# Kernel optimization log

Measured on AMD Instinct MI355X. Metric: run time of the kernel, lower is better.

The kernel has to match this reference:

```python
import jax, jax.numpy as jnp
import numpy as np


def _conv1x1(x, w, b):
    # x: [B, Cin, H, W]; w: [Cout, Cin, 1, 1]; b: [Cout]
    y = jnp.einsum('bchw,oc->bohw', x, w[:, :, 0, 0])
    return y + b[None, :, None, None]


def setup_inputs() -> dict:
    key = jax.random.key(0)
    ks = jax.random.split(key, 9)
    B, C, H, W = 8, 256, 64, 64
    Cq = C // 4
    sc = 0.05
    return {
        'x': jax.random.normal(ks[0], (B, C, H, W), jnp.float32),
        'query_weight': jax.random.normal(ks[1], (Cq, C, 1, 1), jnp.float32) * sc,
        'query_bias': jax.random.normal(ks[2], (Cq,), jnp.float32) * sc,
        'key_weight': jax.random.normal(ks[3], (Cq, C, 1, 1), jnp.float32) * sc,
        'key_bias': jax.random.normal(ks[4], (Cq,), jnp.float32) * sc,
        'value_weight': jax.random.normal(ks[5], (C, C, 1, 1), jnp.float32) * sc,
        'value_bias': jax.random.normal(ks[6], (C,), jnp.float32) * sc,
        'gamma_weight': jax.random.normal(ks[7], (C, C, 1, 1), jnp.float32) * sc,
        'gamma_bias': jax.random.normal(ks[8], (C,), jnp.float32) * sc,
    }


def reference(x, query_weight, query_bias, key_weight, key_bias,
              value_weight, value_bias, gamma_weight, gamma_bias):
    B, C, H, W = x.shape
    N = H * W
    q = _conv1x1(x, query_weight, query_bias).reshape(B, -1, N)   # [B, Cq, N]
    k = _conv1x1(x, key_weight, key_bias).reshape(B, -1, N)       # [B, Cq, N]
    v = _conv1x1(x, value_weight, value_bias).reshape(B, C, N)    # [B, C, N]
    # energy[b, i, j] = sum_c q[b, c, i] * k[b, c, j]
    energy = jnp.einsum('bci,bcj->bij', q, k)                     # [B, N, N]
    energy = jax.nn.elu(energy) / N
    out = jnp.einsum('bcn,bnm->bcm', v, energy).reshape(B, C, H, W)
    return _conv1x1(out, gamma_weight, gamma_bias)
```

## Files before the change

kernel.cpp:

```cpp
#include <hip/hip_runtime.h>
#include <cmath>

#define BB 8
#define CC 256
#define CQ 64
#define NN 4096
constexpr float INV_N = 1.0f / 4096.0f;

typedef __attribute__((ext_vector_type(8))) short short8;
typedef __attribute__((ext_vector_type(4))) short short4v;
typedef __attribute__((ext_vector_type(4))) float float4v;

__device__ __forceinline__ short f2bf(float f) {
  union { float f; unsigned u; } x; x.f = f;
  unsigned r = x.u + 0x7fffu + ((x.u >> 16) & 1u);
  return (short)(r >> 16);
}

__global__ __launch_bounds__(256, 2) void qkv_kernel(
    const float* __restrict__ X,
    const float* __restrict__ wq, const float* __restrict__ bq,
    const float* __restrict__ wk, const float* __restrict__ bk,
    const float* __restrict__ wv, const float* __restrict__ bv,
    short* __restrict__ qt, short* __restrict__ kt, short* __restrict__ vbf) {
  __shared__ short xt[64 * 272];
  __shared__ short Os[64 * 72];
  const int tid = threadIdx.x;
  const int wid = tid >> 6;
  const int lane = tid & 63, quad = lane >> 4, l16 = lane & 15;
  const int n0 = blockIdx.x * 64, b = blockIdx.y;

#pragma unroll 4
  for (int p = 0; p < 16; ++p) {
    const int idx = p * 256 + tid;
    const int c = idx >> 4;
    const int n4 = (idx & 15) * 4;
    const float4 x4 = *reinterpret_cast<const float4*>(
        &X[((size_t)b * CC + c) * NN + n0 + n4]);
    xt[(n4 + 0) * 272 + c] = f2bf(x4.x);
    xt[(n4 + 1) * 272 + c] = f2bf(x4.y);
    xt[(n4 + 2) * 272 + c] = f2bf(x4.z);
    xt[(n4 + 3) * 272 + c] = f2bf(x4.w);
  }
  __syncthreads();

  for (int ch = 0; ch < 6; ++ch) {
    const float* W; const float* bias; int obase;
    if (ch == 0)      { W = wq; bias = bq; obase = 0; }
    else if (ch == 1) { W = wk; bias = bk; obase = 0; }
    else { W = wv + (size_t)(ch - 2) * 64 * CC; bias = bv + (ch - 2) * 64; obase = (ch - 2) * 64; }

    float4v acc[4];
#pragma unroll
    for (int tm = 0; tm < 4; ++tm) acc[tm] = float4v{0.f, 0.f, 0.f, 0.f};

#pragma unroll
    for (int kk = 0; kk < 8; ++kk) {
      const float* wp = &W[(size_t)(wid * 16 + l16) * CC + kk * 32 + quad * 8];
      const float4v w0 = *reinterpret_cast<const float4v*>(wp);
      const float4v w1 = *reinterpret_cast<const float4v*>(wp + 4);
      short8 a;
      a[0] = f2bf(w0[0]); a[1] = f2bf(w0[1]); a[2] = f2bf(w0[2]); a[3] = f2bf(w0[3]);
      a[4] = f2bf(w1[0]); a[5] = f2bf(w1[1]); a[6] = f2bf(w1[2]); a[7] = f2bf(w1[3]);
#pragma unroll
      for (int tm = 0; tm < 4; ++tm) {
        const short8 bfrag = *reinterpret_cast<const short8*>(
            &xt[(tm * 16 + l16) * 272 + kk * 32 + quad * 8]);
        acc[tm] = __builtin_amdgcn_mfma_f32_16x16x32_bf16(a, bfrag, acc[tm], 0, 0, 0);
      }
    }

    if (ch < 2) {
      short* dst = (ch == 0) ? qt : kt;
#pragma unroll
      for (int tm = 0; tm < 4; ++tm) {
        short4v pk;
#pragma unroll
        for (int r = 0; r < 4; ++r)
          pk[r] = f2bf(acc[tm][r] + bias[wid * 16 + quad * 4 + r]);
        *reinterpret_cast<short4v*>(
            &dst[((size_t)b * NN + n0 + tm * 16 + l16) * 64 + wid * 16 + quad * 4]) = pk;
      }
    } else {
      __syncthreads();
#pragma unroll
      for (int tm = 0; tm < 4; ++tm)
#pragma unroll
        for (int r = 0; r < 4; ++r)
          Os[(wid * 16 + quad * 4 + r) * 72 + tm * 16 + l16] =
              f2bf(acc[tm][r] + bias[wid * 16 + quad * 4 + r]);
      __syncthreads();
      const int o = tid >> 2, ng = (tid & 3) * 16;
      const short8 s0 = *reinterpret_cast<const short8*>(&Os[o * 72 + ng]);
      const short8 s1 = *reinterpret_cast<const short8*>(&Os[o * 72 + ng + 8]);
      short* vp = &vbf[((size_t)b * CC + obase + o) * NN + n0 + ng];
      *reinterpret_cast<short8*>(vp) = s0;
      *reinterpret_cast<short8*>(vp + 8) = s1;
    }
  }
}

__global__ __launch_bounds__(256, 2) void attn_kernel(
    const short* __restrict__ qt, const short* __restrict__ kt,
    const short* __restrict__ vbf, const float* __restrict__ Wg,
    const float* __restrict__ bg, float* __restrict__ out) {
  __shared__ short smem[16896];
  short* Es0 = smem;
  short* Es1 = smem + 4608;
  short* Outs = smem;

  const int tid = threadIdx.x;
  const int wid = tid >> 6;
  const int lane = tid & 63, quad = lane >> 4, l16 = lane & 15;
  const int m0 = blockIdx.x * 64, b = blockIdx.y;

  short8 bkf[4][2];
#pragma unroll
  for (int tm = 0; tm < 4; ++tm)
#pragma unroll
    for (int kk = 0; kk < 2; ++kk)
      bkf[tm][kk] = *reinterpret_cast<const short8*>(
          &kt[((size_t)b * NN + m0 + tm * 16 + l16) * 64 + kk * 32 + quad * 8]);

  const short* qrow = &qt[((size_t)b * NN + wid * 16 + l16) * 64 + quad * 8];
  const short* vrow[4];
#pragma unroll
  for (int tc = 0; tc < 4; ++tc)
    vrow[tc] = &vbf[((size_t)b * CC + wid * 64 + tc * 16 + l16) * NN + quad * 8];

  float4v acc[4][4];
#pragma unroll
  for (int i = 0; i < 4; ++i)
#pragma unroll
    for (int j = 0; j < 4; ++j) acc[i][j] = float4v{0.f, 0.f, 0.f, 0.f};

  short8 aq0 = *reinterpret_cast<const short8*>(qrow);
  short8 aq1 = *reinterpret_cast<const short8*>(qrow + 32);

  for (int it = 0; it < 64; ++it) {
    const int nb = it * 64;
    short* Esw = (it & 1) ? Es1 : Es0;

    short8 av[4][2];
#pragma unroll
    for (int tc = 0; tc < 4; ++tc) {
      av[tc][0] = *reinterpret_cast<const short8*>(vrow[tc] + nb);
      av[tc][1] = *reinterpret_cast<const short8*>(vrow[tc] + nb + 32);
    }

    float4v s[4];
#pragma unroll
    for (int tm = 0; tm < 4; ++tm) {
      float4v t = {0.f, 0.f, 0.f, 0.f};
      t = __builtin_amdgcn_mfma_f32_16x16x32_bf16(aq0, bkf[tm][0], t, 0, 0, 0);
      t = __builtin_amdgcn_mfma_f32_16x16x32_bf16(aq1, bkf[tm][1], t, 0, 0, 0);
      s[tm] = t;
    }

    const short8 aq0n = *reinterpret_cast<const short8*>(qrow + (size_t)(it + 1) * 64 * 64);
    const short8 aq1n = *reinterpret_cast<const short8*>(qrow + (size_t)(it + 1) * 64 * 64 + 32);

#pragma unroll
    for (int tm = 0; tm < 4; ++tm) {
      short4v pk;
#pragma unroll
      for (int r = 0; r < 4; ++r) {
        float sv = s[tm][r];
        sv = (sv > 0.f) ? sv : (__expf(sv) - 1.f);
        pk[r] = f2bf(sv * INV_N);
      }
      *reinterpret_cast<short4v*>(
          &Esw[(tm * 16 + l16) * 72 + wid * 16 + quad * 4]) = pk;
    }
    __syncthreads();

#pragma unroll
    for (int tm = 0; tm < 4; ++tm) {
      const short8 be0 = *reinterpret_cast<const short8*>(
          &Esw[(tm * 16 + l16) * 72 + quad * 8]);
      const short8 be1 = *reinterpret_cast<const short8*>(
          &Esw[(tm * 16 + l16) * 72 + 32 + quad * 8]);
#pragma unroll
      for (int tc = 0; tc < 4; ++tc) {
        acc[tc][tm] = __builtin_amdgcn_mfma_f32_16x16x32_bf16(av[tc][0], be0, acc[tc][tm], 0, 0, 0);
        acc[tc][tm] = __builtin_amdgcn_mfma_f32_16x16x32_bf16(av[tc][1], be1, acc[tc][tm], 0, 0, 0);
      }
    }
    aq0 = aq0n; aq1 = aq1n;
  }

  __syncthreads();
#pragma unroll
  for (int tc = 0; tc < 4; ++tc)
#pragma unroll
    for (int tm = 0; tm < 4; ++tm) {
      short4v pk;
#pragma unroll
      for (int r = 0; r < 4; ++r) pk[r] = f2bf(acc[tc][tm][r]);
      *reinterpret_cast<short4v*>(
          &Outs[(tm * 16 + l16) * 264 + wid * 64 + tc * 16 + quad * 4]) = pk;
    }
  __syncthreads();

#pragma unroll
  for (int i = 0; i < 4; ++i)
#pragma unroll
    for (int j = 0; j < 4; ++j) acc[i][j] = float4v{0.f, 0.f, 0.f, 0.f};

  for (int ks8 = 0; ks8 < 8; ++ks8) {
    short8 ag[4];
#pragma unroll
    for (int to = 0; to < 4; ++to) {
      const float* wp =
          &Wg[(size_t)(wid * 64 + to * 16 + l16) * CC + ks8 * 32 + quad * 8];
      const float4v w0 = *reinterpret_cast<const float4v*>(wp);
      const float4v w1 = *reinterpret_cast<const float4v*>(wp + 4);
      short8 a;
      a[0] = f2bf(w0[0]); a[1] = f2bf(w0[1]); a[2] = f2bf(w0[2]); a[3] = f2bf(w0[3]);
      a[4] = f2bf(w1[0]); a[5] = f2bf(w1[1]); a[6] = f2bf(w1[2]); a[7] = f2bf(w1[3]);
      ag[to] = a;
    }
    short8 bo[4];
#pragma unroll
    for (int tm = 0; tm < 4; ++tm)
      bo[tm] = *reinterpret_cast<const short8*>(
          &Outs[(tm * 16 + l16) * 264 + ks8 * 32 + quad * 8]);
#pragma unroll
    for (int to = 0; to < 4; ++to)
#pragma unroll
      for (int tm = 0; tm < 4; ++tm)
        acc[to][tm] =
            __builtin_amdgcn_mfma_f32_16x16x32_bf16(ag[to], bo[tm], acc[to][tm], 0, 0, 0);
  }

#pragma unroll
  for (int to = 0; to < 4; ++to) {
#pragma unroll
    for (int r = 0; r < 4; ++r) {
      const int o = wid * 64 + to * 16 + quad * 4 + r;
      const float bgv = bg[o];
#pragma unroll
      for (int tm = 0; tm < 4; ++tm) {
        out[((size_t)b * CC + o) * NN + m0 + tm * 16 + l16] =
            acc[to][tm][r] + bgv;
      }
    }
  }
}

extern "C" void kernel_launch(void* const* d_in, const int* in_sizes, int n_in,
                              void* d_out, int out_size, void* d_ws,
                              size_t ws_size, hipStream_t stream) {
  const float* x  = (const float*)d_in[0];
  const float* wq = (const float*)d_in[1];
  const float* bq = (const float*)d_in[2];
  const float* wk = (const float*)d_in[3];
  const float* bk = (const float*)d_in[4];
  const float* wv = (const float*)d_in[5];
  const float* bv = (const float*)d_in[6];
  const float* wg = (const float*)d_in[7];
  const float* bg = (const float*)d_in[8];
  float* out = (float*)d_out;

  short* qt  = (short*)d_ws;
  short* kt  = qt + (size_t)BB * NN * CQ;
  short* vbf = kt + (size_t)BB * NN * CQ;

  qkv_kernel<<<dim3(NN / 64, BB), 256, 0, stream>>>(x, wq, bq, wk, bk, wv, bv,
                                                    qt, kt, vbf);
  attn_kernel<<<dim3(NN / 64, BB), 256, 0, stream>>>(qt, kt, vbf, wg, bg, out);
}
```

Baseline: 286.0 us.

## Pre-convert weights to bf16, prefetch V fragments, and swap grid axes

```diff
diff --git a/kernel.cpp b/kernel.cpp
--- a/kernel.cpp
+++ b/kernel.cpp
@@ -17,18 +17,38 @@
   return (short)(r >> 16);
 }
 
+__global__ void wconv_kernel(const float* __restrict__ wq,
+                             const float* __restrict__ wk,
+                             const float* __restrict__ wv,
+                             const float* __restrict__ wg,
+                             short* __restrict__ wqb, short* __restrict__ wkb,
+                             short* __restrict__ wvb, short* __restrict__ wgb) {
+  const int t = blockIdx.x * 256 + threadIdx.x;
+  const float* src;
+  short* dst;
+  int idx;
+  if (t < 4096)        { src = wq; dst = wqb; idx = t; }
+  else if (t < 8192)   { src = wk; dst = wkb; idx = t - 4096; }
+  else if (t < 24576)  { src = wv; dst = wvb; idx = t - 8192; }
+  else                 { src = wg; dst = wgb; idx = t - 24576; }
+  const float4 v = *reinterpret_cast<const float4*>(&src[(size_t)idx * 4]);
+  short4v o;
+  o[0] = f2bf(v.x); o[1] = f2bf(v.y); o[2] = f2bf(v.z); o[3] = f2bf(v.w);
+  *reinterpret_cast<short4v*>(&dst[(size_t)idx * 4]) = o;
+}
+
 __global__ __launch_bounds__(256, 2) void qkv_kernel(
     const float* __restrict__ X,
-    const float* __restrict__ wq, const float* __restrict__ bq,
-    const float* __restrict__ wk, const float* __restrict__ bk,
-    const float* __restrict__ wv, const float* __restrict__ bv,
+    const short* __restrict__ wqb, const float* __restrict__ bq,
+    const short* __restrict__ wkb, const float* __restrict__ bk,
+    const short* __restrict__ wvb, const float* __restrict__ bv,
     short* __restrict__ qt, short* __restrict__ kt, short* __restrict__ vbf) {
   __shared__ short xt[64 * 272];
   __shared__ short Os[64 * 72];
   const int tid = threadIdx.x;
   const int wid = tid >> 6;
   const int lane = tid & 63, quad = lane >> 4, l16 = lane & 15;
-  const int n0 = blockIdx.x * 64, b = blockIdx.y;
+  const int b = blockIdx.x, n0 = blockIdx.y * 64;
 
 #pragma unroll 4
   for (int p = 0; p < 16; ++p) {
@@ -45,29 +65,28 @@
   __syncthreads();
 
   for (int ch = 0; ch < 6; ++ch) {
-    const float* W; const float* bias; int obase;
-    if (ch == 0)      { W = wq; bias = bq; obase = 0; }
-    else if (ch == 1) { W = wk; bias = bk; obase = 0; }
-    else { W = wv + (size_t)(ch - 2) * 64 * CC; bias = bv + (ch - 2) * 64; obase = (ch - 2) * 64; }
+    const short* W; const float* bias; int obase;
+    if (ch == 0)      { W = wqb; bias = bq; obase = 0; }
+    else if (ch == 1) { W = wkb; bias = bk; obase = 0; }
+    else { W = wvb + (size_t)(ch - 2) * 64 * CC; bias = bv + (ch - 2) * 64; obase = (ch - 2) * 64; }
 
     float4v acc[4];
 #pragma unroll
     for (int tm = 0; tm < 4; ++tm) acc[tm] = float4v{0.f, 0.f, 0.f, 0.f};
 
+    const short* wrow = &W[(size_t)(wid * 16 + l16) * CC + quad * 8];
+    short8 a_cur = *reinterpret_cast<const short8*>(wrow);
 #pragma unroll
     for (int kk = 0; kk < 8; ++kk) {
-      const float* wp = &W[(size_t)(wid * 16 + l16) * CC + kk * 32 + quad * 8];
-      const float4v w0 = *reinterpret_cast<const float4v*>(wp);
-      const float4v w1 = *reinterpret_cast<const float4v*>(wp + 4);
-      short8 a;
-      a[0] = f2bf(w0[0]); a[1] = f2bf(w0[1]); a[2] = f2bf(w0[2]); a[3] = f2bf(w0[3]);
-      a[4] = f2bf(w1[0]); a[5] = f2bf(w1[1]); a[6] = f2bf(w1[2]); a[7] = f2bf(w1[3]);
+      short8 a_nxt = a_cur;
+      if (kk < 7) a_nxt = *reinterpret_cast<const short8*>(wrow + (kk + 1) * 32);
 #pragma unroll
       for (int tm = 0; tm < 4; ++tm) {
         const short8 bfrag = *reinterpret_cast<const short8*>(
             &xt[(tm * 16 + l16) * 272 + kk * 32 + quad * 8]);
-        acc[tm] = __builtin_amdgcn_mfma_f32_16x16x32_bf16(a, bfrag, acc[tm], 0, 0, 0);
-      }
+        acc[tm] = __builtin_amdgcn_mfma_f32_16x16x32_bf16(a_cur, bfrag, acc[tm], 0, 0, 0);
+      }
+      a_cur = a_nxt;
     }
 
     if (ch < 2) {
@@ -102,7 +121,7 @@
 
 __global__ __launch_bounds__(256, 2) void attn_kernel(
     const short* __restrict__ qt, const short* __restrict__ kt,
-    const short* __restrict__ vbf, const float* __restrict__ Wg,
+    const short* __restrict__ vbf, const short* __restrict__ wgb,
     const float* __restrict__ bg, float* __restrict__ out) {
   __shared__ short smem[16896];
   short* Es0 = smem;
@@ -112,7 +131,7 @@
   const int tid = threadIdx.x;
   const int wid = tid >> 6;
   const int lane = tid & 63, quad = lane >> 4, l16 = lane & 15;
-  const int m0 = blockIdx.x * 64, b = blockIdx.y;
+  const int b = blockIdx.x, m0 = blockIdx.y * 64;
 
   short8 bkf[4][2];
 #pragma unroll
@@ -136,16 +155,21 @@
 
   short8 aq0 = *reinterpret_cast<const short8*>(qrow);
   short8 aq1 = *reinterpret_cast<const short8*>(qrow + 32);
-
-  for (int it = 0; it < 64; ++it) {
-    const int nb = it * 64;
+  short8 av0[4][2], av1[4][2];
+#pragma unroll
+  for (int tc = 0; tc < 4; ++tc) {
+    av0[tc][0] = *reinterpret_cast<const short8*>(vrow[tc]);
+    av0[tc][1] = *reinterpret_cast<const short8*>(vrow[tc] + 32);
+  }
+
+  auto body = [&](int it, short8 (&avc)[4][2], short8 (&avn)[4][2]) {
     short* Esw = (it & 1) ? Es1 : Es0;
-
-    short8 av[4][2];
+    const int nbn = (it + 1) * 64;
+
 #pragma unroll
     for (int tc = 0; tc < 4; ++tc) {
-      av[tc][0] = *reinterpret_cast<const short8*>(vrow[tc] + nb);
-      av[tc][1] = *reinterpret_cast<const short8*>(vrow[tc] + nb + 32);
+      avn[tc][0] = *reinterpret_cast<const short8*>(vrow[tc] + nbn);
+      avn[tc][1] = *reinterpret_cast<const short8*>(vrow[tc] + nbn + 32);
     }
 
     float4v s[4];
@@ -157,8 +181,8 @@
       s[tm] = t;
     }
 
-    const short8 aq0n = *reinterpret_cast<const short8*>(qrow + (size_t)(it + 1) * 64 * 64);
-    const short8 aq1n = *reinterpret_cast<const short8*>(qrow + (size_t)(it + 1) * 64 * 64 + 32);
+    const short8 aq0n = *reinterpret_cast<const short8*>(qrow + (size_t)nbn * 64);
+    const short8 aq1n = *reinterpret_cast<const short8*>(qrow + (size_t)nbn * 64 + 32);
 
 #pragma unroll
     for (int tm = 0; tm < 4; ++tm) {
@@ -182,11 +206,16 @@
           &Esw[(tm * 16 + l16) * 72 + 32 + quad * 8]);
 #pragma unroll
       for (int tc = 0; tc < 4; ++tc) {
-        acc[tc][tm] = __builtin_amdgcn_mfma_f32_16x16x32_bf16(av[tc][0], be0, acc[tc][tm], 0, 0, 0);
-        acc[tc][tm] = __builtin_amdgcn_mfma_f32_16x16x32_bf16(av[tc][1], be1, acc[tc][tm], 0, 0, 0);
+        acc[tc][tm] = __builtin_amdgcn_mfma_f32_16x16x32_bf16(avc[tc][0], be0, acc[tc][tm], 0, 0, 0);
+        acc[tc][tm] = __builtin_amdgcn_mfma_f32_16x16x32_bf16(avc[tc][1], be1, acc[tc][tm], 0, 0, 0);
       }
     }
     aq0 = aq0n; aq1 = aq1n;
+  };
+
+  for (int it = 0; it < 64; it += 2) {
+    body(it, av0, av1);
+    body(it + 1, av1, av0);
   }
 
   __syncthreads();
@@ -210,16 +239,9 @@
   for (int ks8 = 0; ks8 < 8; ++ks8) {
     short8 ag[4];
 #pragma unroll
-    for (int to = 0; to < 4; ++to) {
-      const float* wp =
-          &Wg[(size_t)(wid * 64 + to * 16 + l16) * CC + ks8 * 32 + quad * 8];
-      const float4v w0 = *reinterpret_cast<const float4v*>(wp);
-      const float4v w1 = *reinterpret_cast<const float4v*>(wp + 4);
-      short8 a;
-      a[0] = f2bf(w0[0]); a[1] = f2bf(w0[1]); a[2] = f2bf(w0[2]); a[3] = f2bf(w0[3]);
-      a[4] = f2bf(w1[0]); a[5] = f2bf(w1[1]); a[6] = f2bf(w1[2]); a[7] = f2bf(w1[3]);
-      ag[to] = a;
-    }
+    for (int to = 0; to < 4; ++to)
+      ag[to] = *reinterpret_cast<const short8*>(
+          &wgb[(size_t)(wid * 64 + to * 16 + l16) * CC + ks8 * 32 + quad * 8]);
     short8 bo[4];
 #pragma unroll
     for (int tm = 0; tm < 4; ++tm)
@@ -265,8 +287,13 @@
   short* qt  = (short*)d_ws;
   short* kt  = qt + (size_t)BB * NN * CQ;
   short* vbf = kt + (size_t)BB * NN * CQ;
-
-  qkv_kernel<<<dim3(NN / 64, BB), 256, 0, stream>>>(x, wq, bq, wk, bk, wv, bv,
+  short* wqb = vbf + (size_t)BB * CC * NN;
+  short* wkb = wqb + (size_t)CQ * CC;
+  short* wvb = wkb + (size_t)CQ * CC;
+  short* wgb = wvb + (size_t)CC * CC;
+
+  wconv_kernel<<<dim3(160), 256, 0, stream>>>(wq, wk, wv, wg, wqb, wkb, wvb, wgb);
+  qkv_kernel<<<dim3(BB, NN / 64), 256, 0, stream>>>(x, wqb, bq, wkb, bk, wvb, bv,
                                                     qt, kt, vbf);
-  attn_kernel<<<dim3(NN / 64, BB), 256, 0, stream>>>(qt, kt, vbf, wg, bg, out);
-}
+  attn_kernel<<<dim3(BB, NN / 64), 256, 0, stream>>>(qt, kt, vbf, wgb, bg, out);
+}
```

Result: faster. 271.2 us (-5.2%).
